# Kernel tuning notes

Hardware: AMD Instinct MI355X
Metric: run time of the kernel (lower is better)

## Reference

```python
import jax, jax.numpy as jnp
import numpy as np

B, C, L = 16, 256, 2048

def setup_inputs() -> dict:
    key = jax.random.key(0)
    y = jax.random.normal(key, (B, C, L), dtype=jnp.float32)
    alpha = jnp.float32(0.5)
    beta = jnp.float32(0.5)
    gamma = jnp.float32(0.0)
    return {"y": y, "alpha": alpha, "beta": beta, "gamma": gamma}

def reference(y, alpha, beta, gamma):
    # y: [B, C, L]
    Bs, Cs, Ls = y.shape
    # channel attention: scores over channels, scaled by 1/sqrt(L)
    scale_c = 1.0 / np.sqrt(max(Ls, 1)).astype(np.float32)
    scores_c = jnp.einsum('bcl,bdl->bcd', y, y) * scale_c          # [B, C, C]
    attn_c = jax.nn.softmax(scores_c, axis=-1)
    y_c = jnp.einsum('bcd,bdl->bcl', attn_c, y)                    # [B, C, L]
    # time attention: scores over time steps, scaled by 1/sqrt(C)
    scale_t = 1.0 / np.sqrt(max(Cs, 1)).astype(np.float32)
    scores_t = jnp.einsum('bcl,bcm->blm', y, y) * scale_t          # [B, L, L]
    attn_t = jax.nn.softmax(scores_t, axis=-1)
    y_t = jnp.einsum('blm,bcm->bcl', attn_t, y)                    # [B, C, L]
    # learnable weighted combine + residual (gamma)
    out = alpha * y_c + beta * y_t + gamma * y
    return out
```

## Files before the change

### kernel.cpp

```cpp
#include <hip/hip_runtime.h>

#define B_ 16
#define C_ 256
#define L_ 2048

typedef __attribute__((ext_vector_type(8))) short short8;
typedef __attribute__((ext_vector_type(4))) float float4v;

__device__ inline float4v mfma16(short8 a, short8 b, float4v c) {
  return __builtin_amdgcn_mfma_f32_16x16x32_bf16(a, b, c, 0, 0, 0);
}

__device__ inline ushort f2bf(float x) {
  union { float f; unsigned u; } v; v.f = x;
  unsigned r = (v.u + 0x7fffu + ((v.u >> 16) & 1u)) >> 16;
  return (ushort)r;
}

__device__ inline float bf2f(ushort u) {
  union { unsigned u; float f; } v; v.u = ((unsigned)u) << 16;
  return v.f;
}

__device__ inline void dma16(const ushort* g, void* l) {
  __builtin_amdgcn_global_load_lds(
      (const __attribute__((address_space(1))) unsigned int*)(g),
      (__attribute__((address_space(3))) unsigned int*)(l), 16, 0, 0);
}

#define BAR_FULL() asm volatile("s_waitcnt vmcnt(0) lgkmcnt(0)\ns_barrier" ::: "memory")
#define BAR_LGKM() asm volatile("s_waitcnt lgkmcnt(0)\ns_barrier" ::: "memory")

__global__ __launch_bounds__(256) void cvt_kernel(const float* __restrict__ y,
                                                  ushort* __restrict__ yb,
                                                  ushort* __restrict__ ytb) {
  __shared__ float tile[32][33];
  int b = blockIdx.z, ct = blockIdx.y, lt = blockIdx.x;
  int tx = threadIdx.x & 31, ty = threadIdx.x >> 5;
  size_t base = ((size_t)b * C_ + (size_t)ct * 32) * L_ + (size_t)lt * 32;
#pragma unroll
  for (int i = 0; i < 4; ++i) {
    int r = ty + i * 8;
    float v = y[base + (size_t)r * L_ + tx];
    tile[r][tx] = v;
    yb[base + (size_t)r * L_ + tx] = f2bf(v);
  }
  __syncthreads();
  size_t tbase = ((size_t)b * L_ + (size_t)lt * 32) * C_ + (size_t)ct * 32;
#pragma unroll
  for (int i = 0; i < 4; ++i) {
    int r = ty + i * 8;
    ytb[tbase + (size_t)r * C_ + tx] = f2bf(tile[tx][r]);
  }
}

__global__ __launch_bounds__(256) void pk_kernel(const ushort* __restrict__ yb,
                                                 ushort* __restrict__ Pc,
                                                 float* __restrict__ ginvC) {
  const int blk = blockIdx.x;
  const int b = (blk & 7) + 8 * ((blk >> 3) & 1);
  const int m0 = (blk >> 4) * 16;
  const int tid = threadIdx.x;
  const int w = tid >> 6, lane = tid & 63, quad = lane >> 4, l16 = lane & 15;
  const float scale = 0.022097086912079608f;
  const float SHIFT = 45.0f;

  __shared__ __align__(16) unsigned char Tb[2][32768];
  __shared__ float wsum[4][16];

  const ushort* Yb = yb + (size_t)b * C_ * L_;
  const int chq = ((lane & 3) - ((lane >> 3) & 3)) & 3;
  const int dl = (lane >> 2) * L_ + chq * 8;
  const int sK = (quad + ((l16 >> 1) & 3)) & 3;
  const int frag_lane = l16 * 64 + sK * 16;

  float4v acc[4];
#pragma unroll
  for (int nt = 0; nt < 4; ++nt) acc[nt] = (float4v){0.f, 0.f, 0.f, 0.f};

#pragma unroll
  for (int j = 0; j < 8; ++j) {
    int gi = w * 8 + j, kk2 = gi >> 4, chgrp = gi & 15;
    dma16(Yb + (size_t)chgrp * 16 * L_ + kk2 * 32 + dl, (void*)(Tb[0] + gi * 1024));
  }

  for (int c = 0; c < 32; ++c) {
    BAR_FULL();
    if (c < 31) {
      int kc = (c + 1) * 64;
      unsigned char* bp = Tb[(c + 1) & 1];
#pragma unroll
      for (int j = 0; j < 8; ++j) {
        int gi = w * 8 + j, kk2 = gi >> 4, chgrp = gi & 15;
        dma16(Yb + (size_t)chgrp * 16 * L_ + kc + kk2 * 32 + dl, (void*)(bp + gi * 1024));
      }
    }
    const unsigned char* cbuf = Tb[c & 1];
#pragma unroll
    for (int kk2 = 0; kk2 < 2; ++kk2) {
      short8 aA = *(const short8*)(cbuf + (kk2 * 16 + (m0 >> 4)) * 1024 + frag_lane);
#pragma unroll
      for (int nt = 0; nt < 4; ++nt) {
        short8 bB = *(const short8*)(cbuf + (kk2 * 16 + w * 4 + nt) * 1024 + frag_lane);
        acc[nt] = mfma16(aA, bB, acc[nt]);
      }
    }
  }

  float p[4][4], rs[4] = {0.f, 0.f, 0.f, 0.f};
#pragma unroll
  for (int nt = 0; nt < 4; ++nt)
#pragma unroll
    for (int r = 0; r < 4; ++r) {
      p[nt][r] = __expf(fmaf(acc[nt][r], scale, -SHIFT));
      rs[r] += p[nt][r];
    }
  ushort* Pb = Pc + ((size_t)b * 256 + m0) * 256;
#pragma unroll
  for (int nt = 0; nt < 4; ++nt)
#pragma unroll
    for (int r = 0; r < 4; ++r)
      Pb[(quad * 4 + r) * 256 + w * 64 + nt * 16 + l16] = f2bf(p[nt][r]);
#pragma unroll
  for (int r = 0; r < 4; ++r)
#pragma unroll
    for (int off = 1; off < 16; off <<= 1) rs[r] += __shfl_xor(rs[r], off);
  if (l16 == 0) {
#pragma unroll
    for (int r = 0; r < 4; ++r) wsum[w][quad * 4 + r] = rs[r];
  }
  __syncthreads();
  if (tid < 16)
    ginvC[b * 256 + m0 + tid] =
        1.0f / (wsum[0][tid] + wsum[1][tid] + wsum[2][tid] + wsum[3][tid]);
}

__global__ __launch_bounds__(256, 2) void ct_kernel(
    const ushort* __restrict__ yb, const ushort* __restrict__ ytb,
    const ushort* __restrict__ Pc, const float* __restrict__ ginvC,
    float* __restrict__ out, const float* __restrict__ alpha_p,
    const float* __restrict__ beta_p, const float* __restrict__ gamma_p) {
  const int blk = blockIdx.x;
  const int b = (blk & 7) + 8 * ((blk >> 3) & 1);
  const int m0 = (blk >> 4) * 64;
  const int tid = threadIdx.x;
  const int w = tid >> 6, lane = tid & 63, quad = lane >> 4, l16 = lane & 15;
  const int mtw = w >> 1, kt2 = w & 1;
  const float scale = 0.0625f;
  const float SHIFT = 16.0f;

  __shared__ __align__(16) unsigned char buf[2][32768];
  __shared__ ushort Pd[64 * 40];
  __shared__ float wsum[4][64];
  __shared__ float ginv[64];

  const ushort* Yt = ytb + (size_t)b * L_ * C_;
  const ushort* Yb = yb + (size_t)b * C_ * L_;
  const ushort* Pcb = Pc + (size_t)b * 256 * 256;
  const int chq = ((lane & 3) - ((lane >> 3) & 3)) & 3;
  const int klK = (lane >> 2) * C_ + chq * 8;
  const int vlV = (lane >> 2) * L_ + chq * 8;
  const int pcl = (lane >> 2) * 256 + chq * 8;
  const int sK = (quad + ((l16 >> 1) & 3)) & 3;
  const int frag_lane = l16 * 64 + sK * 16;

  short8 Qf[2][8];
#pragma unroll
  for (int mt = 0; mt < 2; ++mt)
#pragma unroll
    for (int kk = 0; kk < 8; ++kk)
      Qf[mt][kk] = *(const short8*)(Yt + (size_t)(m0 + mtw * 32 + mt * 16 + l16) * C_ +
                                    kk * 32 + quad * 8);
  const ushort* qgrow[2];
#pragma unroll
  for (int mt = 0; mt < 2; ++mt)
    qgrow[mt] = Yt + (size_t)(m0 + (1 - mtw) * 32 + mt * 16 + l16) * C_ + quad * 8;

  float4v fc[4][4];
#pragma unroll
  for (int mt = 0; mt < 4; ++mt)
#pragma unroll
    for (int nt = 0; nt < 4; ++nt) fc[mt][nt] = (float4v){0.f, 0.f, 0.f, 0.f};

  short8 qg[2][2];
#pragma unroll
  for (int mt = 0; mt < 2; ++mt) qg[0][mt] = *(const short8*)(qgrow[mt]);
#pragma unroll
  for (int j = 0; j < 4; ++j) {
    int gi = w * 4 + j;
    dma16(Pcb + (size_t)(gi * 16) * 256 + pcl, (void*)(buf[0] + gi * 1024));
  }

  for (int c2 = 0; c2 < 8; ++c2) {
    const int cb = c2 & 1;
    BAR_FULL();
    if (c2 < 7) {
      unsigned char* bp = buf[cb ^ 1];
#pragma unroll
      for (int j = 0; j < 4; ++j) {
        int gi = w * 4 + j;
        dma16(Pcb + (size_t)(gi * 16) * 256 + (c2 + 1) * 32 + pcl,
              (void*)(bp + gi * 1024));
      }
#pragma unroll
      for (int mt = 0; mt < 2; ++mt)
        qg[cb ^ 1][mt] = *(const short8*)(qgrow[mt] + (c2 + 1) * 32);
    }
#pragma unroll
    for (int mt = 0; mt < 4; ++mt) {
      short8 Ac = *(const short8*)(buf[cb] + (w * 4 + mt) * 1024 + frag_lane);
#pragma unroll
      for (int nt = 0; nt < 4; ++nt) {
        short8 Bq = ((nt >> 1) == mtw) ? Qf[nt & 1][c2] : qg[cb][nt & 1];
        fc[mt][nt] = mfma16(Ac, Bq, fc[mt][nt]);
      }
    }
  }

  const ushort* dp[8];
#pragma unroll
  for (int j = 0; j < 8; ++j) {
    int gi = w * 8 + j;
    if (gi < 16) {
      int kk = gi >> 1, g = gi & 1;
      dp[j] = Yt + (size_t)(g * 16) * C_ + kk * 32 + klK;
    } else {
      int cg = gi - 16;
      dp[j] = Yb + (size_t)cg * 16 * L_ + vlV;
    }
  }
  const int dstride = (w < 2) ? 32 * C_ : 32;

  float4v ft[4][4];
#pragma unroll
  for (int mt = 0; mt < 4; ++mt)
#pragma unroll
    for (int nt = 0; nt < 4; ++nt) ft[mt][nt] = (float4v){0.f, 0.f, 0.f, 0.f};
  float rs[2][4] = {{0.f, 0.f, 0.f, 0.f}, {0.f, 0.f, 0.f, 0.f}};

#pragma unroll
  for (int j = 0; j < 8; ++j) {
    dma16(dp[j], (void*)(buf[0] + (w * 8 + j) * 1024));
    dp[j] += dstride;
  }

  for (int c = 0; c < 64; ++c) {
    const int cb = c & 1;
    BAR_FULL();
    if (c < 63) {
      unsigned char* bp = buf[cb ^ 1];
#pragma unroll
      for (int j = 0; j < 8; ++j) {
        dma16(dp[j], (void*)(bp + (w * 8 + j) * 1024));
        dp[j] += dstride;
      }
    }
    float4v s0 = (float4v){0.f, 0.f, 0.f, 0.f};
    float4v s1 = (float4v){0.f, 0.f, 0.f, 0.f};
#pragma unroll
    for (int kk = 0; kk < 8; ++kk) {
      short8 bf = *(const short8*)(buf[cb] + (kk * 2 + kt2) * 1024 + frag_lane);
      s0 = mfma16(Qf[0][kk], bf, s0);
      s1 = mfma16(Qf[1][kk], bf, s1);
    }
#pragma unroll
    for (int mt = 0; mt < 2; ++mt) {
      float4v s = mt ? s1 : s0;
#pragma unroll
      for (int r = 0; r < 4; ++r) {
        float p = __expf(fmaf(s[r], scale, -SHIFT));
        rs[mt][r] += p;
        Pd[(mtw * 32 + mt * 16 + quad * 4 + r) * 40 + kt2 * 16 + l16] = f2bf(p);
      }
    }
    BAR_LGKM();
#pragma unroll
    for (int mt = 0; mt < 4; ++mt) {
      short8 va = *(const short8*)(buf[cb] + (16 + w * 4 + mt) * 1024 + frag_lane);
#pragma unroll
      for (int nt = 0; nt < 4; ++nt) {
        short8 pb = *(const short8*)(&Pd[(nt * 16 + l16) * 40 + quad * 8]);
        ft[mt][nt] = mfma16(va, pb, ft[mt][nt]);
      }
    }
  }

  __syncthreads();
#pragma unroll
  for (int mt = 0; mt < 2; ++mt)
#pragma unroll
    for (int r = 0; r < 4; ++r)
#pragma unroll
      for (int off = 1; off < 16; off <<= 1) rs[mt][r] += __shfl_xor(rs[mt][r], off);
  if (l16 == 0) {
#pragma unroll
    for (int mt = 0; mt < 2; ++mt)
#pragma unroll
      for (int r = 0; r < 4; ++r)
        wsum[w][mtw * 32 + mt * 16 + quad * 4 + r] = rs[mt][r];
  }
  __syncthreads();
  if (tid < 64) {
    int mh = tid >> 5;
    ginv[tid] = 1.0f / (wsum[mh * 2][tid] + wsum[mh * 2 + 1][tid]);
  }
  __syncthreads();

  const float alpha = alpha_p[0], beta = beta_p[0], gamma = gamma_p[0];
  float gq[4];
#pragma unroll
  for (int nt = 0; nt < 4; ++nt) gq[nt] = beta * ginv[nt * 16 + l16];
  float gc[4][4];
#pragma unroll
  for (int mt = 0; mt < 4; ++mt)
#pragma unroll
    for (int r = 0; r < 4; ++r)
      gc[mt][r] = alpha * ginvC[b * 256 + w * 64 + mt * 16 + quad * 4 + r];

  if (gamma != 0.0f) {
#pragma unroll
    for (int mt = 0; mt < 4; ++mt)
#pragma unroll
      for (int nt = 0; nt < 4; ++nt)
#pragma unroll
        for (int r = 0; r < 4; ++r) {
          int ch = w * 64 + mt * 16 + quad * 4 + r;
          size_t idx = ((size_t)b * C_ + ch) * L_ + m0 + nt * 16 + l16;
          float v = gc[mt][r] * fc[mt][nt][r] + gq[nt] * ft[mt][nt][r];
          out[idx] = fmaf(gamma, bf2f(Yb[(size_t)ch * L_ + m0 + nt * 16 + l16]), v);
        }
  } else {
#pragma unroll
    for (int mt = 0; mt < 4; ++mt)
#pragma unroll
      for (int nt = 0; nt < 4; ++nt)
#pragma unroll
        for (int r = 0; r < 4; ++r) {
          int ch = w * 64 + mt * 16 + quad * 4 + r;
          size_t idx = ((size_t)b * C_ + ch) * L_ + m0 + nt * 16 + l16;
          out[idx] = gc[mt][r] * fc[mt][nt][r] + gq[nt] * ft[mt][nt][r];
        }
  }
}

extern "C" void kernel_launch(void* const* d_in, const int* in_sizes, int n_in,
                              void* d_out, int out_size, void* d_ws, size_t ws_size,
                              hipStream_t stream) {
  const float* y = (const float*)d_in[0];
  const float* alpha = (const float*)d_in[1];
  const float* beta = (const float*)d_in[2];
  const float* gamma = (const float*)d_in[3];
  float* out = (float*)d_out;

  ushort* yb = (ushort*)d_ws;
  ushort* ytb = yb + (size_t)B_ * C_ * L_;
  ushort* Pc = ytb + (size_t)B_ * C_ * L_;
  float* ginvC = (float*)(Pc + (size_t)B_ * 256 * 256);

  hipLaunchKernelGGL(cvt_kernel, dim3(L_ / 32, C_ / 32, B_), dim3(256), 0, stream,
                     y, yb, ytb);
  hipLaunchKernelGGL(pk_kernel, dim3(256), dim3(256), 0, stream, yb, Pc, ginvC);
  hipLaunchKernelGGL(ct_kernel, dim3(512), dim3(256), 0, stream,
                     yb, ytb, Pc, ginvC, out, alpha, beta, gamma);
}
```

Measured before the change: 216.8 us.

## Deepen DMA pipelining, widen cvt tiles, and add MFMA priority hints

The conversion kernel now uses 64x64 tiles with float4 loads and ushort4 stores. The channel-score kernel moves to 512 threads with a three-stage DMA ring and partial vmcnt waits. The main kernel's time loop issues the next-next chunk's DMA after compute and waits with vmcnt(8), so loads can overlap more. s_setprio is raised around the MFMA blocks. This aims to cut load-latency stalls and improve conversion bandwidth, at the cost of extra barriers and more LDS in pk_kernel.

```diff
diff --git a/kernel.cpp b/kernel.cpp
--- a/kernel.cpp
+++ b/kernel.cpp
@@ -30,31 +30,42 @@
 
 #define BAR_FULL() asm volatile("s_waitcnt vmcnt(0) lgkmcnt(0)\ns_barrier" ::: "memory")
 #define BAR_LGKM() asm volatile("s_waitcnt lgkmcnt(0)\ns_barrier" ::: "memory")
+#define BAR_VM8() asm volatile("s_waitcnt vmcnt(8)\ns_barrier" ::: "memory")
+#define BAR_VM4() asm volatile("s_waitcnt vmcnt(4)\ns_barrier" ::: "memory")
+#define BAR_VM0() asm volatile("s_waitcnt vmcnt(0)\ns_barrier" ::: "memory")
+#define BAR_RAW() asm volatile("s_barrier" ::: "memory")
 
 __global__ __launch_bounds__(256) void cvt_kernel(const float* __restrict__ y,
                                                   ushort* __restrict__ yb,
                                                   ushort* __restrict__ ytb) {
-  __shared__ float tile[32][33];
+  __shared__ float tile[64][68];
   int b = blockIdx.z, ct = blockIdx.y, lt = blockIdx.x;
-  int tx = threadIdx.x & 31, ty = threadIdx.x >> 5;
-  size_t base = ((size_t)b * C_ + (size_t)ct * 32) * L_ + (size_t)lt * 32;
+  int tx = threadIdx.x & 15, ty = threadIdx.x >> 4;
+  size_t base = ((size_t)b * C_ + (size_t)ct * 64) * L_ + (size_t)lt * 64;
 #pragma unroll
   for (int i = 0; i < 4; ++i) {
-    int r = ty + i * 8;
-    float v = y[base + (size_t)r * L_ + tx];
-    tile[r][tx] = v;
-    yb[base + (size_t)r * L_ + tx] = f2bf(v);
-  }
-  __syncthreads();
-  size_t tbase = ((size_t)b * L_ + (size_t)lt * 32) * C_ + (size_t)ct * 32;
+    int r = ty + i * 16;
+    float4 v = *(const float4*)(y + base + (size_t)r * L_ + tx * 4);
+    *(float4*)(&tile[r][tx * 4]) = v;
+    ushort4 u;
+    u.x = f2bf(v.x); u.y = f2bf(v.y); u.z = f2bf(v.z); u.w = f2bf(v.w);
+    *(ushort4*)(yb + base + (size_t)r * L_ + tx * 4) = u;
+  }
+  __syncthreads();
+  size_t tbase = ((size_t)b * L_ + (size_t)lt * 64) * C_ + (size_t)ct * 64;
 #pragma unroll
   for (int i = 0; i < 4; ++i) {
-    int r = ty + i * 8;
-    ytb[tbase + (size_t)r * C_ + tx] = f2bf(tile[tx][r]);
-  }
-}
-
-__global__ __launch_bounds__(256) void pk_kernel(const ushort* __restrict__ yb,
+    int r = ty + i * 16;
+    ushort4 u;
+    u.x = f2bf(tile[tx * 4 + 0][r]);
+    u.y = f2bf(tile[tx * 4 + 1][r]);
+    u.z = f2bf(tile[tx * 4 + 2][r]);
+    u.w = f2bf(tile[tx * 4 + 3][r]);
+    *(ushort4*)(ytb + tbase + (size_t)r * C_ + tx * 4) = u;
+  }
+}
+
+__global__ __launch_bounds__(512) void pk_kernel(const ushort* __restrict__ yb,
                                                  ushort* __restrict__ Pc,
                                                  float* __restrict__ ginvC) {
   const int blk = blockIdx.x;
@@ -65,8 +76,8 @@
   const float scale = 0.022097086912079608f;
   const float SHIFT = 45.0f;
 
-  __shared__ __align__(16) unsigned char Tb[2][32768];
-  __shared__ float wsum[4][16];
+  __shared__ __align__(16) unsigned char Tb[3][32768];
+  __shared__ float wsum[8][16];
 
   const ushort* Yb = yb + (size_t)b * C_ * L_;
   const int chq = ((lane & 3) - ((lane >> 3) & 3)) & 3;
@@ -74,42 +85,43 @@
   const int sK = (quad + ((l16 >> 1) & 3)) & 3;
   const int frag_lane = l16 * 64 + sK * 16;
 
-  float4v acc[4];
-#pragma unroll
-  for (int nt = 0; nt < 4; ++nt) acc[nt] = (float4v){0.f, 0.f, 0.f, 0.f};
-
-#pragma unroll
-  for (int j = 0; j < 8; ++j) {
-    int gi = w * 8 + j, kk2 = gi >> 4, chgrp = gi & 15;
-    dma16(Yb + (size_t)chgrp * 16 * L_ + kk2 * 32 + dl, (void*)(Tb[0] + gi * 1024));
-  }
+  float4v acc[2];
+#pragma unroll
+  for (int nt = 0; nt < 2; ++nt) acc[nt] = (float4v){0.f, 0.f, 0.f, 0.f};
+
+  auto PK_STAGE = [&](int t) {
+    int kc = t * 64;
+    unsigned char* bp = Tb[t % 3];
+#pragma unroll
+    for (int j = 0; j < 4; ++j) {
+      int gi = w * 4 + j, kk2 = gi >> 4, chgrp = gi & 15;
+      dma16(Yb + (size_t)chgrp * 16 * L_ + kc + kk2 * 32 + dl, (void*)(bp + gi * 1024));
+    }
+  };
+
+  PK_STAGE(0);
+  PK_STAGE(1);
 
   for (int c = 0; c < 32; ++c) {
-    BAR_FULL();
-    if (c < 31) {
-      int kc = (c + 1) * 64;
-      unsigned char* bp = Tb[(c + 1) & 1];
-#pragma unroll
-      for (int j = 0; j < 8; ++j) {
-        int gi = w * 8 + j, kk2 = gi >> 4, chgrp = gi & 15;
-        dma16(Yb + (size_t)chgrp * 16 * L_ + kc + kk2 * 32 + dl, (void*)(bp + gi * 1024));
-      }
-    }
-    const unsigned char* cbuf = Tb[c & 1];
+    if (c == 31) { BAR_VM0(); } else { BAR_VM4(); }
+    if (c < 30) PK_STAGE(c + 2);
+    const unsigned char* cbuf = Tb[c % 3];
+    __builtin_amdgcn_s_setprio(1);
 #pragma unroll
     for (int kk2 = 0; kk2 < 2; ++kk2) {
       short8 aA = *(const short8*)(cbuf + (kk2 * 16 + (m0 >> 4)) * 1024 + frag_lane);
 #pragma unroll
-      for (int nt = 0; nt < 4; ++nt) {
-        short8 bB = *(const short8*)(cbuf + (kk2 * 16 + w * 4 + nt) * 1024 + frag_lane);
+      for (int nt = 0; nt < 2; ++nt) {
+        short8 bB = *(const short8*)(cbuf + (kk2 * 16 + w * 2 + nt) * 1024 + frag_lane);
         acc[nt] = mfma16(aA, bB, acc[nt]);
       }
     }
-  }
-
-  float p[4][4], rs[4] = {0.f, 0.f, 0.f, 0.f};
-#pragma unroll
-  for (int nt = 0; nt < 4; ++nt)
+    __builtin_amdgcn_s_setprio(0);
+  }
+
+  float p[2][4], rs[4] = {0.f, 0.f, 0.f, 0.f};
+#pragma unroll
+  for (int nt = 0; nt < 2; ++nt)
 #pragma unroll
     for (int r = 0; r < 4; ++r) {
       p[nt][r] = __expf(fmaf(acc[nt][r], scale, -SHIFT));
@@ -117,10 +129,10 @@
     }
   ushort* Pb = Pc + ((size_t)b * 256 + m0) * 256;
 #pragma unroll
-  for (int nt = 0; nt < 4; ++nt)
+  for (int nt = 0; nt < 2; ++nt)
 #pragma unroll
     for (int r = 0; r < 4; ++r)
-      Pb[(quad * 4 + r) * 256 + w * 64 + nt * 16 + l16] = f2bf(p[nt][r]);
+      Pb[(quad * 4 + r) * 256 + w * 32 + nt * 16 + l16] = f2bf(p[nt][r]);
 #pragma unroll
   for (int r = 0; r < 4; ++r)
 #pragma unroll
@@ -130,9 +142,12 @@
     for (int r = 0; r < 4; ++r) wsum[w][quad * 4 + r] = rs[r];
   }
   __syncthreads();
-  if (tid < 16)
-    ginvC[b * 256 + m0 + tid] =
-        1.0f / (wsum[0][tid] + wsum[1][tid] + wsum[2][tid] + wsum[3][tid]);
+  if (tid < 16) {
+    float s = 0.f;
+#pragma unroll
+    for (int ww = 0; ww < 8; ++ww) s += wsum[ww][tid];
+    ginvC[b * 256 + m0 + tid] = 1.0f / s;
+  }
 }
 
 __global__ __launch_bounds__(256, 2) void ct_kernel(
@@ -206,6 +221,7 @@
       for (int mt = 0; mt < 2; ++mt)
         qg[cb ^ 1][mt] = *(const short8*)(qgrow[mt] + (c2 + 1) * 32);
     }
+    __builtin_amdgcn_s_setprio(1);
 #pragma unroll
     for (int mt = 0; mt < 4; ++mt) {
       short8 Ac = *(const short8*)(buf[cb] + (w * 4 + mt) * 1024 + frag_lane);
@@ -215,6 +231,7 @@
         fc[mt][nt] = mfma16(Ac, Bq, fc[mt][nt]);
       }
     }
+    __builtin_amdgcn_s_setprio(0);
   }
 
   const ushort* dp[8];
@@ -243,26 +260,26 @@
     dma16(dp[j], (void*)(buf[0] + (w * 8 + j) * 1024));
     dp[j] += dstride;
   }
+  BAR_RAW();
+#pragma unroll
+  for (int j = 0; j < 8; ++j) {
+    dma16(dp[j], (void*)(buf[1] + (w * 8 + j) * 1024));
+    dp[j] += dstride;
+  }
 
   for (int c = 0; c < 64; ++c) {
     const int cb = c & 1;
-    BAR_FULL();
-    if (c < 63) {
-      unsigned char* bp = buf[cb ^ 1];
-#pragma unroll
-      for (int j = 0; j < 8; ++j) {
-        dma16(dp[j], (void*)(bp + (w * 8 + j) * 1024));
-        dp[j] += dstride;
-      }
-    }
+    if (c == 63) { BAR_VM0(); } else { BAR_VM8(); }
     float4v s0 = (float4v){0.f, 0.f, 0.f, 0.f};
     float4v s1 = (float4v){0.f, 0.f, 0.f, 0.f};
+    __builtin_amdgcn_s_setprio(1);
 #pragma unroll
     for (int kk = 0; kk < 8; ++kk) {
       short8 bf = *(const short8*)(buf[cb] + (kk * 2 + kt2) * 1024 + frag_lane);
       s0 = mfma16(Qf[0][kk], bf, s0);
       s1 = mfma16(Qf[1][kk], bf, s1);
     }
+    __builtin_amdgcn_s_setprio(0);
 #pragma unroll
     for (int mt = 0; mt < 2; ++mt) {
       float4v s = mt ? s1 : s0;
@@ -274,6 +291,7 @@
       }
     }
     BAR_LGKM();
+    __builtin_amdgcn_s_setprio(1);
 #pragma unroll
     for (int mt = 0; mt < 4; ++mt) {
       short8 va = *(const short8*)(buf[cb] + (16 + w * 4 + mt) * 1024 + frag_lane);
@@ -281,6 +299,15 @@
       for (int nt = 0; nt < 4; ++nt) {
         short8 pb = *(const short8*)(&Pd[(nt * 16 + l16) * 40 + quad * 8]);
         ft[mt][nt] = mfma16(va, pb, ft[mt][nt]);
+      }
+    }
+    __builtin_amdgcn_s_setprio(0);
+    BAR_RAW();
+    if (c < 62) {
+#pragma unroll
+      for (int j = 0; j < 8; ++j) {
+        dma16(dp[j], (void*)(buf[cb] + (w * 8 + j) * 1024));
+        dp[j] += dstride;
       }
     }
   }
@@ -357,9 +384,9 @@
   ushort* Pc = ytb + (size_t)B_ * C_ * L_;
   float* ginvC = (float*)(Pc + (size_t)B_ * 256 * 256);
 
-  hipLaunchKernelGGL(cvt_kernel, dim3(L_ / 32, C_ / 32, B_), dim3(256), 0, stream,
+  hipLaunchKernelGGL(cvt_kernel, dim3(L_ / 64, C_ / 64, B_), dim3(256), 0, stream,
                      y, yb, ytb);
-  hipLaunchKernelGGL(pk_kernel, dim3(256), dim3(256), 0, stream, yb, Pc, ginvC);
+  hipLaunchKernelGGL(pk_kernel, dim3(256), dim3(512), 0, stream, yb, Pc, ginvC);
   hipLaunchKernelGGL(ct_kernel, dim3(512), dim3(256), 0, stream,
                      yb, ytb, Pc, ginvC, out, alpha, beta, gamma);
 }
```

Result: faster. 205.1 us (-5.4%).
